# Optimization experiments

Measured on AMD Instinct MI355X. Metric: run time of the kernel, lower is better.

## Reference

```python
import jax, jax.numpy as jnp
import numpy as np

INV_SQRT2 = 0.7071067811865476  # ResidualLayer scale in GemNet
SILU_SCALE = 1.0 / 0.6          # ScaledSiLU scale factor


def scaled_silu(x):
    return jax.nn.silu(x) * SILU_SCALE


def setup_inputs() -> dict:
    key = jax.random.key(0)
    ks = jax.random.split(key, 9)
    E, A, D, NB = 200000, 10000, 256, 5  # edges, atoms, emb_size_edge, int_blocks+1

    def w(k, shape):
        fan_in = shape[0]
        return jax.random.normal(k, shape, jnp.float32) * (2.0 / fan_in) ** 0.5

    return {
        "x_cat": jax.random.normal(ks[0], (E, D * NB), jnp.float32),
        "edge_vec": jax.random.normal(ks[1], (E, 3), jnp.float32),
        "edge_idx": jax.random.randint(ks[2], (E,), 0, A),
        "W_in": w(ks[3], (D * NB, D)),
        "W_r1a": w(ks[4], (D, D)),
        "W_r1b": w(ks[5], (D, D)),
        "W_r2a": w(ks[6], (D, D)),
        "W_r2b": w(ks[7], (D, D)),
        "W_out": w(ks[8], (D, 1)),
        "n_atoms": A,
    }


def reference(x_cat, edge_vec, edge_idx, W_in, W_r1a, W_r1b, W_r2a, W_r2b, W_out, n_atoms):
    # out_mlp_F: Dense(in->emb) + 2 residual layers (all Dense are bias-free + ScaledSiLU)
    x = scaled_silu(x_cat @ W_in)                                   # [E, D]
    x = (x + scaled_silu(scaled_silu(x @ W_r1a) @ W_r1b)) * INV_SQRT2
    x = (x + scaled_silu(scaled_silu(x @ W_r2a) @ W_r2b)) * INV_SQRT2
    # out_forces: Dense(D -> 1, bias=False, no activation)
    F_st = x @ W_out                                                # [E, 1]
    # F_st_vec = F_st[:, :, None] * edge_vec[:, None, :] -> squeeze the size-1 dim
    F_vec = F_st * edge_vec                                         # [E, 3]
    # scatter_add over target atom index
    forces = jax.ops.segment_sum(F_vec, edge_idx, num_segments=n_atoms)  # [A, 3]
    return forces
```

## Files before the change

### kernel.cpp

```cpp
#include <hip/hip_runtime.h>

typedef __attribute__((ext_vector_type(4))) float f32x4;
typedef __attribute__((ext_vector_type(8))) __bf16 bf16x8;
typedef __attribute__((ext_vector_type(8))) unsigned short us8;
typedef unsigned short u16;

#define SSILU_SCALE (1.0f / 0.6f)
#define INV_SQRT2 0.70710678118654752f

__device__ __forceinline__ u16 f2bf(float f) {
    __bf16 h = (__bf16)f;
    return __builtin_bit_cast(u16, h);
}
__device__ __forceinline__ float bf2f(u16 h) {
    union { unsigned int u; float f; } v; v.u = ((unsigned int)h) << 16;
    return v.f;
}
__device__ __forceinline__ float ssilu(float x) {
    float e = __expf(-x);
    float s = __builtin_amdgcn_rcpf(1.0f + e);
    return x * s * SSILU_SCALE;
}

__global__ __launch_bounds__(256) void prep_kernel(
    const float* __restrict__ Win, const float* __restrict__ W1a,
    const float* __restrict__ W1b, const float* __restrict__ W2a,
    const float* __restrict__ W2b, u16* __restrict__ WinF,
    u16* __restrict__ Wfrag, float* __restrict__ out, int outN) {
    int i = blockIdx.x * 256 + threadIdx.x;
    if (i < 327680) {
        int e = i & 7, lane = (i >> 3) & 63, n = (i >> 9) & 3;
        int kk = (i >> 11) & 1, w = (i >> 12) & 3, kt = i >> 14;
        int lo = lane & 15, hi = lane >> 4;
        int k = kt * 64 + kk * 32 + hi * 8 + e;
        int col = w * 64 + n * 16 + lo;
        WinF[i] = f2bf(Win[k * 256 + col]);
        return;
    }
    int j = i - 327680;
    if (j < 262144) {
        int g = j >> 16, r = j & 65535;
        int chunk = r >> 9, within = r & 511;
        int lane = within >> 3, e = within & 7;
        int w = chunk >> 5, kk = (chunk >> 2) & 7, n = chunk & 3;
        int lo = lane & 15, hi = lane >> 4;
        int col = w * 64 + n * 16 + lo;
        int k = kk * 32 + hi * 8 + e;
        const float* W = (g == 0) ? W1a : (g == 1) ? W1b : (g == 2) ? W2a : W2b;
        Wfrag[j] = f2bf(W[k * 256 + col]);
        return;
    }
    int z = j - 262144;
    if (z < outN) out[z] = 0.0f;
}

__device__ __forceinline__ void gemm_lds(const char* AB, const u16* __restrict__ Wfw,
                                         int l, int lo, int hi, f32x4 acc[4][4]) {
#pragma unroll
    for (int m = 0; m < 4; m++)
#pragma unroll
        for (int n = 0; n < 4; n++) acc[m][n] = (f32x4){0.f, 0.f, 0.f, 0.f};
    bf16x8 bv[4];
#pragma unroll
    for (int n = 0; n < 4; n++)
        bv[n] = __builtin_bit_cast(bf16x8,
            *(const us8*)(Wfw + (size_t)n * 512 + l * 8));
#pragma unroll
    for (int kk = 0; kk < 8; ++kk) {
        int kbyte = kk * 64 + hi * 16;
        bf16x8 af[4], bvn[4];
#pragma unroll
        for (int m = 0; m < 4; m++) {
            int r = m * 16 + lo;
            af[m] = __builtin_bit_cast(bf16x8,
                *(const us8*)(AB + r * 512 + (kbyte ^ ((r & 7) << 4))));
        }
        if (kk < 7) {
#pragma unroll
            for (int n = 0; n < 4; n++)
                bvn[n] = __builtin_bit_cast(bf16x8,
                    *(const us8*)(Wfw + (size_t)((kk + 1) * 4 + n) * 512 + l * 8));
        }
#pragma unroll
        for (int m = 0; m < 4; m++)
#pragma unroll
            for (int n = 0; n < 4; n++)
                acc[m][n] = __builtin_amdgcn_mfma_f32_16x16x32_bf16(
                    af[m], bv[n], acc[m][n], 0, 0, 0);
        if (kk < 7) {
#pragma unroll
            for (int n = 0; n < 4; n++) bv[n] = bvn[n];
        }
    }
}

__global__ __launch_bounds__(256, 2) void fused_kernel(
    const float* __restrict__ A, const u16* __restrict__ WinF,
    const u16* __restrict__ Wfrag, const float* __restrict__ Wout,
    const float* __restrict__ evec, const int* __restrict__ eidx,
    float* __restrict__ out) {
    __shared__ u16 xb[64 * 256];
    __shared__ u16 tb[64 * 256];
    __shared__ float fpart[4][64];
    const int t = threadIdx.x, w = t >> 6, l = t & 63;
    const int lo = l & 15, hi = l >> 4;
    const long rowbase = (long)blockIdx.x * 64;
    char* xbB = (char*)xb;
    char* tbB = (char*)tb;
    char* As0 = (char*)tb;
    char* As1 = (char*)tb + 8192;

    f32x4 acc[4][4];
#pragma unroll
    for (int m = 0; m < 4; m++)
#pragma unroll
        for (int n = 0; n < 4; n++) acc[m][n] = (f32x4){0.f, 0.f, 0.f, 0.f};

    float4 va[2][2];
    auto LOADA = [&](int kb) {
#pragma unroll
        for (int c = 0; c < 2; ++c) {
            int idx = t + c * 256;
            int r = idx >> 3, k8 = (idx & 7) * 8;
            const float* s = A + (rowbase + r) * 1280 + kb + k8;
            va[c][0] = *(const float4*)s;
            va[c][1] = *(const float4*)(s + 4);
        }
    };
    auto WRITEA = [&](char* dst) {
#pragma unroll
        for (int c = 0; c < 2; ++c) {
            int idx = t + c * 256;
            int r = idx >> 3, k8 = (idx & 7) * 8;
            us8 p;
            p[0] = f2bf(va[c][0].x); p[1] = f2bf(va[c][0].y);
            p[2] = f2bf(va[c][0].z); p[3] = f2bf(va[c][0].w);
            p[4] = f2bf(va[c][1].x); p[5] = f2bf(va[c][1].y);
            p[6] = f2bf(va[c][1].z); p[7] = f2bf(va[c][1].w);
            *(us8*)(dst + r * 128 + ((k8 * 2) ^ ((r & 7) << 4))) = p;
        }
    };
    auto LOADB = [&](int kt, bf16x8 (&b)[8]) {
        const u16* base = WinF + kt * 16384 + w * 4096 + l * 8;
#pragma unroll
        for (int kk = 0; kk < 2; ++kk)
#pragma unroll
            for (int n = 0; n < 4; ++n)
                b[kk * 4 + n] = __builtin_bit_cast(bf16x8,
                    *(const us8*)(base + kk * 2048 + n * 512));
    };

    bf16x8 b0[8], b1[8];

    auto STEP = [&](int kt, const char* ABcur, char* ABnxt,
                    bf16x8 (&bc)[8], bf16x8 (&bn)[8]) {
        const bool more = (kt + 1 < 20);
        if (more) {
            LOADA((kt + 1) * 64);
            LOADB(kt + 1, bn);
        }
#pragma unroll
        for (int kk = 0; kk < 2; ++kk) {
            int kbyte = kk * 64 + hi * 16;
            bf16x8 af[4];
#pragma unroll
            for (int m = 0; m < 4; m++) {
                int r = m * 16 + lo;
                af[m] = __builtin_bit_cast(bf16x8,
                    *(const us8*)(ABcur + r * 128 + (kbyte ^ ((r & 7) << 4))));
            }
#pragma unroll
            for (int m = 0; m < 4; m++)
#pragma unroll
                for (int n = 0; n < 4; n++)
                    acc[m][n] = __builtin_amdgcn_mfma_f32_16x16x32_bf16(
                        af[m], bc[kk * 4 + n], acc[m][n], 0, 0, 0);
        }
        if (more) WRITEA(ABnxt);
        asm volatile("s_waitcnt lgkmcnt(0)" ::: "memory");
        __builtin_amdgcn_sched_barrier(0);
        __builtin_amdgcn_s_barrier();
    };

    LOADA(0);
    LOADB(0, b0);
    WRITEA(As0);
    asm volatile("s_waitcnt lgkmcnt(0)" ::: "memory");
    __builtin_amdgcn_s_barrier();

    for (int i = 0; i < 10; ++i) {
        STEP(2 * i,     As0, As1, b0, b1);
        STEP(2 * i + 1, As1, As0, b1, b0);
    }

#pragma unroll
    for (int m = 0; m < 4; m++)
#pragma unroll
        for (int n = 0; n < 4; n++)
#pragma unroll
            for (int j = 0; j < 4; j++) {
                int r = m * 16 + hi * 4 + j;
                int cc = w * 64 + n * 16 + lo;
                *(u16*)(xbB + r * 512 + ((cc * 2) ^ ((r & 7) << 4))) =
                    f2bf(ssilu(acc[m][n][j]));
            }
    __syncthreads();

    const u16* Wfw = Wfrag + w * 16384;

    gemm_lds(xbB, Wfw + 0 * 65536, l, lo, hi, acc);
#pragma unroll
    for (int m = 0; m < 4; m++)
#pragma unroll
        for (int n = 0; n < 4; n++)
#pragma unroll
            for (int j = 0; j < 4; j++) {
                int r = m * 16 + hi * 4 + j;
                int cc = w * 64 + n * 16 + lo;
                *(u16*)(tbB + r * 512 + ((cc * 2) ^ ((r & 7) << 4))) =
                    f2bf(ssilu(acc[m][n][j]));
            }
    __syncthreads();

    gemm_lds(tbB, Wfw + 1 * 65536, l, lo, hi, acc);
#pragma unroll
    for (int m = 0; m < 4; m++)
#pragma unroll
        for (int n = 0; n < 4; n++)
#pragma unroll
            for (int j = 0; j < 4; j++) {
                int r = m * 16 + hi * 4 + j;
                int cc = w * 64 + n * 16 + lo;
                char* p = xbB + r * 512 + ((cc * 2) ^ ((r & 7) << 4));
                float xn = (bf2f(*(u16*)p) + ssilu(acc[m][n][j])) * INV_SQRT2;
                *(u16*)p = f2bf(xn);
            }
    __syncthreads();

    gemm_lds(xbB, Wfw + 2 * 65536, l, lo, hi, acc);
#pragma unroll
    for (int m = 0; m < 4; m++)
#pragma unroll
        for (int n = 0; n < 4; n++)
#pragma unroll
            for (int j = 0; j < 4; j++) {
                int r = m * 16 + hi * 4 + j;
                int cc = w * 64 + n * 16 + lo;
                *(u16*)(tbB + r * 512 + ((cc * 2) ^ ((r & 7) << 4))) =
                    f2bf(ssilu(acc[m][n][j]));
            }
    __syncthreads();

    gemm_lds(tbB, Wfw + 3 * 65536, l, lo, hi, acc);
    float wo[4];
#pragma unroll
    for (int n = 0; n < 4; n++) wo[n] = Wout[w * 64 + n * 16 + lo];

    float part[4][4];
#pragma unroll
    for (int m = 0; m < 4; m++)
#pragma unroll
        for (int j = 0; j < 4; j++) part[m][j] = 0.f;
#pragma unroll
    for (int m = 0; m < 4; m++)
#pragma unroll
        for (int n = 0; n < 4; n++)
#pragma unroll
            for (int j = 0; j < 4; j++) {
                int r = m * 16 + hi * 4 + j;
                int cc = w * 64 + n * 16 + lo;
                const char* p = xbB + r * 512 + ((cc * 2) ^ ((r & 7) << 4));
                float xf = (bf2f(*(const u16*)p) + ssilu(acc[m][n][j])) * INV_SQRT2;
                part[m][j] += xf * wo[n];
            }
#pragma unroll
    for (int m = 0; m < 4; m++)
#pragma unroll
        for (int j = 0; j < 4; j++) {
            float v = part[m][j];
            v += __shfl_xor(v, 1);
            v += __shfl_xor(v, 2);
            v += __shfl_xor(v, 4);
            v += __shfl_xor(v, 8);
            if (lo == 0) fpart[w][m * 16 + hi * 4 + j] = v;
        }
    __syncthreads();

    if (t < 64) {
        int r = t;
        float F = fpart[0][r] + fpart[1][r] + fpart[2][r] + fpart[3][r];
        long e = rowbase + r;
        float vx = evec[e * 3 + 0], vy = evec[e * 3 + 1], vz = evec[e * 3 + 2];
        int a = eidx[e];
        atomicAdd(&out[a * 3 + 0], F * vx);
        atomicAdd(&out[a * 3 + 1], F * vy);
        atomicAdd(&out[a * 3 + 2], F * vz);
    }
}

extern "C" void kernel_launch(void* const* d_in, const int* in_sizes, int n_in,
                              void* d_out, int out_size, void* d_ws, size_t ws_size,
                              hipStream_t stream) {
    const float* x_cat = (const float*)d_in[0];
    const float* evec  = (const float*)d_in[1];
    const int*   eidx  = (const int*)d_in[2];
    const float* Win   = (const float*)d_in[3];
    const float* W1a   = (const float*)d_in[4];
    const float* W1b   = (const float*)d_in[5];
    const float* W2a   = (const float*)d_in[6];
    const float* W2b   = (const float*)d_in[7];
    const float* Wout  = (const float*)d_in[8];
    float* out = (float*)d_out;
    const int E = in_sizes[1] / 3;

    u16* WinF  = (u16*)d_ws;
    u16* Wfrag = WinF + 327680;

    int prepN = 327680 + 262144 + out_size;
    prep_kernel<<<(prepN + 255) / 256, 256, 0, stream>>>(
        Win, W1a, W1b, W2a, W2b, WinF, Wfrag, out, out_size);
    fused_kernel<<<E / 64, 256, 0, stream>>>(
        x_cat, WinF, Wfrag, Wout, evec, eidx, out);
}
```

Baseline: 406.2 us.

## Split fused MLP across 8 waves and deepen A-tile global prefetch

The fused kernel now uses 512 threads (8 waves) per 64-row tile, with each wave owning 32 output columns instead of 64. This halves accumulator and B-fragment registers per wave and adds more waves per CU to hide latency. The first GEMM's K loop is restructured into a software pipeline that keeps two A tiles in flight in registers ahead of the LDS write, hiding more of the global load latency. The trade-off is more waves contending for the same LDS tiles and barriers, and duplicated A-fragment LDS reads across the wave pairs.

```diff
diff --git a/kernel.cpp b/kernel.cpp
--- a/kernel.cpp
+++ b/kernel.cpp
@@ -54,111 +54,95 @@
     if (z < outN) out[z] = 0.0f;
 }
 
-__device__ __forceinline__ void gemm_lds(const char* AB, const u16* __restrict__ Wfw,
-                                         int l, int lo, int hi, f32x4 acc[4][4]) {
-#pragma unroll
-    for (int m = 0; m < 4; m++)
-#pragma unroll
-        for (int n = 0; n < 4; n++) acc[m][n] = (f32x4){0.f, 0.f, 0.f, 0.f};
-    bf16x8 bv[4];
-#pragma unroll
-    for (int n = 0; n < 4; n++)
-        bv[n] = __builtin_bit_cast(bf16x8,
-            *(const us8*)(Wfw + (size_t)n * 512 + l * 8));
+__device__ __forceinline__ void gemm_lds8(const char* AB, const u16* __restrict__ Wfw,
+                                          int swz, int hi, int lo, f32x4 acc[4][2]) {
+#pragma unroll
+    for (int m = 0; m < 4; m++)
+#pragma unroll
+        for (int n = 0; n < 2; n++) acc[m][n] = (f32x4){0.f, 0.f, 0.f, 0.f};
+    bf16x8 bv[2], bvn[2];
+#pragma unroll
+    for (int n = 0; n < 2; n++)
+        bv[n] = __builtin_bit_cast(bf16x8, *(const us8*)(Wfw + n * 512));
 #pragma unroll
     for (int kk = 0; kk < 8; ++kk) {
         int kbyte = kk * 64 + hi * 16;
-        bf16x8 af[4], bvn[4];
+        bf16x8 af[4];
 #pragma unroll
         for (int m = 0; m < 4; m++) {
             int r = m * 16 + lo;
             af[m] = __builtin_bit_cast(bf16x8,
-                *(const us8*)(AB + r * 512 + (kbyte ^ ((r & 7) << 4))));
+                *(const us8*)(AB + r * 512 + (kbyte ^ swz)));
         }
         if (kk < 7) {
 #pragma unroll
-            for (int n = 0; n < 4; n++)
+            for (int n = 0; n < 2; n++)
                 bvn[n] = __builtin_bit_cast(bf16x8,
-                    *(const us8*)(Wfw + (size_t)((kk + 1) * 4 + n) * 512 + l * 8));
+                    *(const us8*)(Wfw + (kk + 1) * 2048 + n * 512));
         }
 #pragma unroll
         for (int m = 0; m < 4; m++)
 #pragma unroll
-            for (int n = 0; n < 4; n++)
+            for (int n = 0; n < 2; n++)
                 acc[m][n] = __builtin_amdgcn_mfma_f32_16x16x32_bf16(
                     af[m], bv[n], acc[m][n], 0, 0, 0);
         if (kk < 7) {
 #pragma unroll
-            for (int n = 0; n < 4; n++) bv[n] = bvn[n];
-        }
-    }
-}
-
-__global__ __launch_bounds__(256, 2) void fused_kernel(
+            for (int n = 0; n < 2; n++) bv[n] = bvn[n];
+        }
+    }
+}
+
+__global__ __launch_bounds__(512, 4) void fused_kernel(
     const float* __restrict__ A, const u16* __restrict__ WinF,
     const u16* __restrict__ Wfrag, const float* __restrict__ Wout,
     const float* __restrict__ evec, const int* __restrict__ eidx,
     float* __restrict__ out) {
     __shared__ u16 xb[64 * 256];
     __shared__ u16 tb[64 * 256];
-    __shared__ float fpart[4][64];
+    __shared__ float fpart[8][64];
     const int t = threadIdx.x, w = t >> 6, l = t & 63;
     const int lo = l & 15, hi = l >> 4;
+    const int swz = (lo & 7) << 4;
     const long rowbase = (long)blockIdx.x * 64;
     char* xbB = (char*)xb;
     char* tbB = (char*)tb;
-    char* As0 = (char*)tb;
-    char* As1 = (char*)tb + 8192;
-
-    f32x4 acc[4][4];
-#pragma unroll
-    for (int m = 0; m < 4; m++)
-#pragma unroll
-        for (int n = 0; n < 4; n++) acc[m][n] = (f32x4){0.f, 0.f, 0.f, 0.f};
-
-    float4 va[2][2];
-    auto LOADA = [&](int kb) {
-#pragma unroll
-        for (int c = 0; c < 2; ++c) {
-            int idx = t + c * 256;
-            int r = idx >> 3, k8 = (idx & 7) * 8;
-            const float* s = A + (rowbase + r) * 1280 + kb + k8;
-            va[c][0] = *(const float4*)s;
-            va[c][1] = *(const float4*)(s + 4);
-        }
-    };
-    auto WRITEA = [&](char* dst) {
-#pragma unroll
-        for (int c = 0; c < 2; ++c) {
-            int idx = t + c * 256;
-            int r = idx >> 3, k8 = (idx & 7) * 8;
-            us8 p;
-            p[0] = f2bf(va[c][0].x); p[1] = f2bf(va[c][0].y);
-            p[2] = f2bf(va[c][0].z); p[3] = f2bf(va[c][0].w);
-            p[4] = f2bf(va[c][1].x); p[5] = f2bf(va[c][1].y);
-            p[6] = f2bf(va[c][1].z); p[7] = f2bf(va[c][1].w);
-            *(us8*)(dst + r * 128 + ((k8 * 2) ^ ((r & 7) << 4))) = p;
-        }
-    };
-    auto LOADB = [&](int kt, bf16x8 (&b)[8]) {
-        const u16* base = WinF + kt * 16384 + w * 4096 + l * 8;
+    char* As0 = tbB;
+    char* As1 = tbB + 8192;
+
+    f32x4 acc[4][2];
+#pragma unroll
+    for (int m = 0; m < 4; m++)
+#pragma unroll
+        for (int n = 0; n < 2; n++) acc[m][n] = (f32x4){0.f, 0.f, 0.f, 0.f};
+
+    const int ar = t >> 3, ak8 = (t & 7) * 8;
+    const int awz = ((ak8 * 2) ^ ((ar & 7) << 4));
+    float4 va0[2], va1[2];
+    auto LOADA = [&](int kb, float4* va) {
+        const float* s = A + (rowbase + ar) * 1280 + kb + ak8;
+        va[0] = *(const float4*)s;
+        va[1] = *(const float4*)(s + 4);
+    };
+    auto WRITEA = [&](char* dst, const float4* va) {
+        us8 p;
+        p[0] = f2bf(va[0].x); p[1] = f2bf(va[0].y);
+        p[2] = f2bf(va[0].z); p[3] = f2bf(va[0].w);
+        p[4] = f2bf(va[1].x); p[5] = f2bf(va[1].y);
+        p[6] = f2bf(va[1].z); p[7] = f2bf(va[1].w);
+        *(us8*)(dst + ar * 128 + awz) = p;
+    };
+    const u16* WinFw = WinF + (w >> 1) * 4096 + (w & 1) * 1024 + l * 8;
+    auto LOADB = [&](int kt, bf16x8 (&b)[4]) {
+        const u16* base = WinFw + kt * 16384;
 #pragma unroll
         for (int kk = 0; kk < 2; ++kk)
 #pragma unroll
-            for (int n = 0; n < 4; ++n)
-                b[kk * 4 + n] = __builtin_bit_cast(bf16x8,
+            for (int n = 0; n < 2; ++n)
+                b[kk * 2 + n] = __builtin_bit_cast(bf16x8,
                     *(const us8*)(base + kk * 2048 + n * 512));
     };
-
-    bf16x8 b0[8], b1[8];
-
-    auto STEP = [&](int kt, const char* ABcur, char* ABnxt,
-                    bf16x8 (&bc)[8], bf16x8 (&bn)[8]) {
-        const bool more = (kt + 1 < 20);
-        if (more) {
-            LOADA((kt + 1) * 64);
-            LOADB(kt + 1, bn);
-        }
+    auto MFMASTEP = [&](const char* AB, const bf16x8 (&bc)[4]) {
 #pragma unroll
         for (int kk = 0; kk < 2; ++kk) {
             int kbyte = kk * 64 + hi * 16;
@@ -167,94 +151,129 @@
             for (int m = 0; m < 4; m++) {
                 int r = m * 16 + lo;
                 af[m] = __builtin_bit_cast(bf16x8,
-                    *(const us8*)(ABcur + r * 128 + (kbyte ^ ((r & 7) << 4))));
+                    *(const us8*)(AB + r * 128 + (kbyte ^ swz)));
             }
 #pragma unroll
             for (int m = 0; m < 4; m++)
 #pragma unroll
-                for (int n = 0; n < 4; n++)
+                for (int n = 0; n < 2; n++)
                     acc[m][n] = __builtin_amdgcn_mfma_f32_16x16x32_bf16(
-                        af[m], bc[kk * 4 + n], acc[m][n], 0, 0, 0);
-        }
-        if (more) WRITEA(ABnxt);
+                        af[m], bc[kk * 2 + n], acc[m][n], 0, 0, 0);
+        }
+    };
+    auto FENCE = [&]() {
         asm volatile("s_waitcnt lgkmcnt(0)" ::: "memory");
         __builtin_amdgcn_sched_barrier(0);
         __builtin_amdgcn_s_barrier();
     };
 
-    LOADA(0);
+    bf16x8 b0[4], b1[4];
+
+    LOADA(0, va1);
+    WRITEA(As0, va1);
     LOADB(0, b0);
-    WRITEA(As0);
-    asm volatile("s_waitcnt lgkmcnt(0)" ::: "memory");
-    __builtin_amdgcn_s_barrier();
-
-    for (int i = 0; i < 10; ++i) {
-        STEP(2 * i,     As0, As1, b0, b1);
-        STEP(2 * i + 1, As1, As0, b1, b0);
-    }
-
-#pragma unroll
-    for (int m = 0; m < 4; m++)
-#pragma unroll
-        for (int n = 0; n < 4; n++)
-#pragma unroll
-            for (int j = 0; j < 4; j++) {
-                int r = m * 16 + hi * 4 + j;
-                int cc = w * 64 + n * 16 + lo;
+    LOADA(64, va0);
+    LOADA(128, va1);
+    FENCE();
+
+    for (int i = 0; i < 8; ++i) {
+        const int kt = 2 * i;
+        LOADB(kt + 1, b1);
+        __builtin_amdgcn_sched_barrier(0);
+        MFMASTEP(As0, b0);
+        WRITEA(As1, va0);
+        LOADA((kt + 3) * 64, va0);
+        FENCE();
+        LOADB(kt + 2, b0);
+        __builtin_amdgcn_sched_barrier(0);
+        MFMASTEP(As1, b1);
+        WRITEA(As0, va1);
+        LOADA((kt + 4) * 64, va1);
+        FENCE();
+    }
+    LOADB(17, b1);
+    __builtin_amdgcn_sched_barrier(0);
+    MFMASTEP(As0, b0);
+    WRITEA(As1, va0);
+    LOADA(19 * 64, va0);
+    FENCE();
+
+    LOADB(18, b0);
+    __builtin_amdgcn_sched_barrier(0);
+    MFMASTEP(As1, b1);
+    WRITEA(As0, va1);
+    FENCE();
+
+    LOADB(19, b1);
+    __builtin_amdgcn_sched_barrier(0);
+    MFMASTEP(As0, b0);
+    WRITEA(As1, va0);
+    FENCE();
+
+    MFMASTEP(As1, b1);
+
+#pragma unroll
+    for (int m = 0; m < 4; m++)
+#pragma unroll
+        for (int n = 0; n < 2; n++)
+#pragma unroll
+            for (int j = 0; j < 4; j++) {
+                int r = m * 16 + hi * 4 + j;
+                int cc = w * 32 + n * 16 + lo;
                 *(u16*)(xbB + r * 512 + ((cc * 2) ^ ((r & 7) << 4))) =
                     f2bf(ssilu(acc[m][n][j]));
             }
     __syncthreads();
 
-    const u16* Wfw = Wfrag + w * 16384;
-
-    gemm_lds(xbB, Wfw + 0 * 65536, l, lo, hi, acc);
-#pragma unroll
-    for (int m = 0; m < 4; m++)
-#pragma unroll
-        for (int n = 0; n < 4; n++)
-#pragma unroll
-            for (int j = 0; j < 4; j++) {
-                int r = m * 16 + hi * 4 + j;
-                int cc = w * 64 + n * 16 + lo;
+    const u16* Wfw = Wfrag + (w >> 1) * 16384 + (w & 1) * 1024 + l * 8;
+
+    gemm_lds8(xbB, Wfw + 0 * 65536, swz, hi, lo, acc);
+#pragma unroll
+    for (int m = 0; m < 4; m++)
+#pragma unroll
+        for (int n = 0; n < 2; n++)
+#pragma unroll
+            for (int j = 0; j < 4; j++) {
+                int r = m * 16 + hi * 4 + j;
+                int cc = w * 32 + n * 16 + lo;
                 *(u16*)(tbB + r * 512 + ((cc * 2) ^ ((r & 7) << 4))) =
                     f2bf(ssilu(acc[m][n][j]));
             }
     __syncthreads();
 
-    gemm_lds(tbB, Wfw + 1 * 65536, l, lo, hi, acc);
-#pragma unroll
-    for (int m = 0; m < 4; m++)
-#pragma unroll
-        for (int n = 0; n < 4; n++)
-#pragma unroll
-            for (int j = 0; j < 4; j++) {
-                int r = m * 16 + hi * 4 + j;
-                int cc = w * 64 + n * 16 + lo;
+    gemm_lds8(tbB, Wfw + 1 * 65536, swz, hi, lo, acc);
+#pragma unroll
+    for (int m = 0; m < 4; m++)
+#pragma unroll
+        for (int n = 0; n < 2; n++)
+#pragma unroll
+            for (int j = 0; j < 4; j++) {
+                int r = m * 16 + hi * 4 + j;
+                int cc = w * 32 + n * 16 + lo;
                 char* p = xbB + r * 512 + ((cc * 2) ^ ((r & 7) << 4));
                 float xn = (bf2f(*(u16*)p) + ssilu(acc[m][n][j])) * INV_SQRT2;
                 *(u16*)p = f2bf(xn);
             }
     __syncthreads();
 
-    gemm_lds(xbB, Wfw + 2 * 65536, l, lo, hi, acc);
-#pragma unroll
-    for (int m = 0; m < 4; m++)
-#pragma unroll
-        for (int n = 0; n < 4; n++)
-#pragma unroll
-            for (int j = 0; j < 4; j++) {
-                int r = m * 16 + hi * 4 + j;
-                int cc = w * 64 + n * 16 + lo;
+    gemm_lds8(xbB, Wfw + 2 * 65536, swz, hi, lo, acc);
+#pragma unroll
+    for (int m = 0; m < 4; m++)
+#pragma unroll
+        for (int n = 0; n < 2; n++)
+#pragma unroll
+            for (int j = 0; j < 4; j++) {
+                int r = m * 16 + hi * 4 + j;
+                int cc = w * 32 + n * 16 + lo;
                 *(u16*)(tbB + r * 512 + ((cc * 2) ^ ((r & 7) << 4))) =
                     f2bf(ssilu(acc[m][n][j]));
             }
     __syncthreads();
 
-    gemm_lds(tbB, Wfw + 3 * 65536, l, lo, hi, acc);
-    float wo[4];
-#pragma unroll
-    for (int n = 0; n < 4; n++) wo[n] = Wout[w * 64 + n * 16 + lo];
+    gemm_lds8(tbB, Wfw + 3 * 65536, swz, hi, lo, acc);
+    float wo[2];
+#pragma unroll
+    for (int n = 0; n < 2; n++) wo[n] = Wout[w * 32 + n * 16 + lo];
 
     float part[4][4];
 #pragma unroll
@@ -264,11 +283,11 @@
 #pragma unroll
     for (int m = 0; m < 4; m++)
 #pragma unroll
-        for (int n = 0; n < 4; n++)
-#pragma unroll
-            for (int j = 0; j < 4; j++) {
-                int r = m * 16 + hi * 4 + j;
-                int cc = w * 64 + n * 16 + lo;
+        for (int n = 0; n < 2; n++)
+#pragma unroll
+            for (int j = 0; j < 4; j++) {
+                int r = m * 16 + hi * 4 + j;
+                int cc = w * 32 + n * 16 + lo;
                 const char* p = xbB + r * 512 + ((cc * 2) ^ ((r & 7) << 4));
                 float xf = (bf2f(*(const u16*)p) + ssilu(acc[m][n][j])) * INV_SQRT2;
                 part[m][j] += xf * wo[n];
@@ -288,7 +307,8 @@
 
     if (t < 64) {
         int r = t;
-        float F = fpart[0][r] + fpart[1][r] + fpart[2][r] + fpart[3][r];
+        float F = fpart[0][r] + fpart[1][r] + fpart[2][r] + fpart[3][r] +
+                  fpart[4][r] + fpart[5][r] + fpart[6][r] + fpart[7][r];
         long e = rowbase + r;
         float vx = evec[e * 3 + 0], vy = evec[e * 3 + 1], vz = evec[e * 3 + 2];
         int a = eidx[e];
@@ -319,6 +339,6 @@
     int prepN = 327680 + 262144 + out_size;
     prep_kernel<<<(prepN + 255) / 256, 256, 0, stream>>>(
         Win, W1a, W1b, W2a, W2b, WinF, Wfrag, out, out_size);
-    fused_kernel<<<E / 64, 256, 0, stream>>>(
+    fused_kernel<<<E / 64, 512, 0, stream>>>(
         x_cat, WinF, Wfrag, Wout, evec, eidx, out);
 }
```

After: 423.3 us. +4.2%, slower.

## Halve rows per block to 32 and raise occupancy with finer-grained B prefetch

Applied to the files above, without the earlier changes.

Cuts the per-block edge tile from 64 to 32 rows, which halves the accumulators and LDS buffers. That lets launch bounds request 4 blocks per CU instead of 2. The first GEMM's pipeline now prefetches weight fragments per k-substep and loads A two tiles ahead. The aim is more latency hiding through higher occupancy. The cost is that each block reuses the weights over half as many rows, so per-block weight traffic from L2 roughly doubles relative to compute.

```diff
diff --git a/kernel.cpp b/kernel.cpp
--- a/kernel.cpp
+++ b/kernel.cpp
@@ -55,12 +55,12 @@
 }
 
 __device__ __forceinline__ void gemm_lds(const char* AB, const u16* __restrict__ Wfw,
-                                         int l, int lo, int hi, f32x4 acc[4][4]) {
-#pragma unroll
-    for (int m = 0; m < 4; m++)
+                                         int l, int lo, int hi, f32x4 acc[2][4]) {
+#pragma unroll
+    for (int m = 0; m < 2; m++)
 #pragma unroll
         for (int n = 0; n < 4; n++) acc[m][n] = (f32x4){0.f, 0.f, 0.f, 0.f};
-    bf16x8 bv[4];
+    bf16x8 bv[4], bvn[4];
 #pragma unroll
     for (int n = 0; n < 4; n++)
         bv[n] = __builtin_bit_cast(bf16x8,
@@ -68,9 +68,9 @@
 #pragma unroll
     for (int kk = 0; kk < 8; ++kk) {
         int kbyte = kk * 64 + hi * 16;
-        bf16x8 af[4], bvn[4];
-#pragma unroll
-        for (int m = 0; m < 4; m++) {
+        bf16x8 af[2];
+#pragma unroll
+        for (int m = 0; m < 2; m++) {
             int r = m * 16 + lo;
             af[m] = __builtin_bit_cast(bf16x8,
                 *(const us8*)(AB + r * 512 + (kbyte ^ ((r & 7) << 4))));
@@ -82,7 +82,7 @@
                     *(const us8*)(Wfw + (size_t)((kk + 1) * 4 + n) * 512 + l * 8));
         }
 #pragma unroll
-        for (int m = 0; m < 4; m++)
+        for (int m = 0; m < 2; m++)
 #pragma unroll
             for (int n = 0; n < 4; n++)
                 acc[m][n] = __builtin_amdgcn_mfma_f32_16x16x32_bf16(
@@ -94,107 +94,100 @@
     }
 }
 
-__global__ __launch_bounds__(256, 2) void fused_kernel(
+__global__ __launch_bounds__(256, 4) void fused_kernel(
     const float* __restrict__ A, const u16* __restrict__ WinF,
     const u16* __restrict__ Wfrag, const float* __restrict__ Wout,
     const float* __restrict__ evec, const int* __restrict__ eidx,
     float* __restrict__ out) {
-    __shared__ u16 xb[64 * 256];
-    __shared__ u16 tb[64 * 256];
-    __shared__ float fpart[4][64];
+    __shared__ u16 xb[32 * 256];
+    __shared__ u16 tb[32 * 256];
+    __shared__ float fpart[4][32];
     const int t = threadIdx.x, w = t >> 6, l = t & 63;
     const int lo = l & 15, hi = l >> 4;
-    const long rowbase = (long)blockIdx.x * 64;
+    const int swz = (lo & 7) << 4;
+    const long rowbase = (long)blockIdx.x * 32;
     char* xbB = (char*)xb;
     char* tbB = (char*)tb;
-    char* As0 = (char*)tb;
-    char* As1 = (char*)tb + 8192;
-
-    f32x4 acc[4][4];
-#pragma unroll
-    for (int m = 0; m < 4; m++)
+    char* As0 = tbB;
+    char* As1 = tbB + 4096;
+
+    f32x4 acc[2][4];
+#pragma unroll
+    for (int m = 0; m < 2; m++)
 #pragma unroll
         for (int n = 0; n < 4; n++) acc[m][n] = (f32x4){0.f, 0.f, 0.f, 0.f};
 
-    float4 va[2][2];
+    const int ar = t >> 3, ak8 = (t & 7) * 8;
+    const int awz = ((ak8 * 2) ^ ((ar & 7) << 4));
+    float4 va[2];
     auto LOADA = [&](int kb) {
-#pragma unroll
-        for (int c = 0; c < 2; ++c) {
-            int idx = t + c * 256;
-            int r = idx >> 3, k8 = (idx & 7) * 8;
-            const float* s = A + (rowbase + r) * 1280 + kb + k8;
-            va[c][0] = *(const float4*)s;
-            va[c][1] = *(const float4*)(s + 4);
-        }
+        const float* s = A + (rowbase + ar) * 1280 + kb + ak8;
+        va[0] = *(const float4*)s;
+        va[1] = *(const float4*)(s + 4);
     };
     auto WRITEA = [&](char* dst) {
-#pragma unroll
-        for (int c = 0; c < 2; ++c) {
-            int idx = t + c * 256;
-            int r = idx >> 3, k8 = (idx & 7) * 8;
-            us8 p;
-            p[0] = f2bf(va[c][0].x); p[1] = f2bf(va[c][0].y);
-            p[2] = f2bf(va[c][0].z); p[3] = f2bf(va[c][0].w);
-            p[4] = f2bf(va[c][1].x); p[5] = f2bf(va[c][1].y);
-            p[6] = f2bf(va[c][1].z); p[7] = f2bf(va[c][1].w);
-            *(us8*)(dst + r * 128 + ((k8 * 2) ^ ((r & 7) << 4))) = p;
-        }
-    };
-    auto LOADB = [&](int kt, bf16x8 (&b)[8]) {
-        const u16* base = WinF + kt * 16384 + w * 4096 + l * 8;
-#pragma unroll
-        for (int kk = 0; kk < 2; ++kk)
-#pragma unroll
-            for (int n = 0; n < 4; ++n)
-                b[kk * 4 + n] = __builtin_bit_cast(bf16x8,
-                    *(const us8*)(base + kk * 2048 + n * 512));
-    };
-
-    bf16x8 b0[8], b1[8];
-
-    auto STEP = [&](int kt, const char* ABcur, char* ABnxt,
-                    bf16x8 (&bc)[8], bf16x8 (&bn)[8]) {
-        const bool more = (kt + 1 < 20);
-        if (more) {
-            LOADA((kt + 1) * 64);
-            LOADB(kt + 1, bn);
-        }
-#pragma unroll
-        for (int kk = 0; kk < 2; ++kk) {
-            int kbyte = kk * 64 + hi * 16;
-            bf16x8 af[4];
-#pragma unroll
-            for (int m = 0; m < 4; m++) {
-                int r = m * 16 + lo;
-                af[m] = __builtin_bit_cast(bf16x8,
-                    *(const us8*)(ABcur + r * 128 + (kbyte ^ ((r & 7) << 4))));
-            }
-#pragma unroll
-            for (int m = 0; m < 4; m++)
-#pragma unroll
-                for (int n = 0; n < 4; n++)
-                    acc[m][n] = __builtin_amdgcn_mfma_f32_16x16x32_bf16(
-                        af[m], bc[kk * 4 + n], acc[m][n], 0, 0, 0);
-        }
-        if (more) WRITEA(ABnxt);
+        us8 p;
+        p[0] = f2bf(va[0].x); p[1] = f2bf(va[0].y);
+        p[2] = f2bf(va[0].z); p[3] = f2bf(va[0].w);
+        p[4] = f2bf(va[1].x); p[5] = f2bf(va[1].y);
+        p[6] = f2bf(va[1].z); p[7] = f2bf(va[1].w);
+        *(us8*)(dst + ar * 128 + awz) = p;
+    };
+    const u16* WinFw = WinF + w * 4096 + l * 8;
+    auto LOADB = [&](int kt, int kk, bf16x8 (&b)[4]) {
+        const u16* base = WinFw + kt * 16384 + kk * 2048;
+#pragma unroll
+        for (int n = 0; n < 4; ++n)
+            b[n] = __builtin_bit_cast(bf16x8, *(const us8*)(base + n * 512));
+    };
+    auto MFMA_KK = [&](const char* AB, int kk, const bf16x8 (&bc)[4]) {
+        int kbyte = kk * 64 + hi * 16;
+        bf16x8 af[2];
+#pragma unroll
+        for (int m = 0; m < 2; m++) {
+            int r = m * 16 + lo;
+            af[m] = __builtin_bit_cast(bf16x8,
+                *(const us8*)(AB + r * 128 + (kbyte ^ swz)));
+        }
+#pragma unroll
+        for (int m = 0; m < 2; m++)
+#pragma unroll
+            for (int n = 0; n < 4; n++)
+                acc[m][n] = __builtin_amdgcn_mfma_f32_16x16x32_bf16(
+                    af[m], bc[n], acc[m][n], 0, 0, 0);
+    };
+    auto FENCE = [&]() {
         asm volatile("s_waitcnt lgkmcnt(0)" ::: "memory");
         __builtin_amdgcn_sched_barrier(0);
         __builtin_amdgcn_s_barrier();
     };
 
+    bf16x8 bc[4], bn[4];
+
     LOADA(0);
-    LOADB(0, b0);
     WRITEA(As0);
-    asm volatile("s_waitcnt lgkmcnt(0)" ::: "memory");
-    __builtin_amdgcn_s_barrier();
+    LOADB(0, 0, bc);
+    LOADA(64);
+    FENCE();
+
+    auto STEP = [&](int kt, const char* AScur, char* ASnxt) {
+        const bool more = (kt < 19);
+        LOADB(kt, 1, bn);
+        MFMA_KK(AScur, 0, bc);
+        if (more) LOADB(kt + 1, 0, bc);
+        MFMA_KK(AScur, 1, bn);
+        if (more) WRITEA(ASnxt);
+        if (kt <= 17) LOADA((kt + 2) * 64);
+        FENCE();
+    };
 
     for (int i = 0; i < 10; ++i) {
-        STEP(2 * i,     As0, As1, b0, b1);
-        STEP(2 * i + 1, As1, As0, b1, b0);
-    }
-
-#pragma unroll
-    for (int m = 0; m < 4; m++)
+        STEP(2 * i,     As0, As1);
+        STEP(2 * i + 1, As1, As0);
+    }
+
+#pragma unroll
+    for (int m = 0; m < 2; m++)
 #pragma unroll
         for (int n = 0; n < 4; n++)
 #pragma unroll
@@ -210,7 +203,7 @@
 
     gemm_lds(xbB, Wfw + 0 * 65536, l, lo, hi, acc);
 #pragma unroll
-    for (int m = 0; m < 4; m++)
+    for (int m = 0; m < 2; m++)
 #pragma unroll
         for (int n = 0; n < 4; n++)
 #pragma unroll
@@ -224,7 +217,7 @@
 
     gemm_lds(tbB, Wfw + 1 * 65536, l, lo, hi, acc);
 #pragma unroll
-    for (int m = 0; m < 4; m++)
+    for (int m = 0; m < 2; m++)
 #pragma unroll
         for (int n = 0; n < 4; n++)
 #pragma unroll
@@ -239,7 +232,7 @@
 
     gemm_lds(xbB, Wfw + 2 * 65536, l, lo, hi, acc);
 #pragma unroll
-    for (int m = 0; m < 4; m++)
+    for (int m = 0; m < 2; m++)
 #pragma unroll
         for (int n = 0; n < 4; n++)
 #pragma unroll
@@ -256,13 +249,13 @@
 #pragma unroll
     for (int n = 0; n < 4; n++) wo[n] = Wout[w * 64 + n * 16 + lo];
 
-    float part[4][4];
-#pragma unroll
-    for (int m = 0; m < 4; m++)
+    float part[2][4];
+#pragma unroll
+    for (int m = 0; m < 2; m++)
 #pragma unroll
         for (int j = 0; j < 4; j++) part[m][j] = 0.f;
 #pragma unroll
-    for (int m = 0; m < 4; m++)
+    for (int m = 0; m < 2; m++)
 #pragma unroll
         for (int n = 0; n < 4; n++)
 #pragma unroll
@@ -274,7 +267,7 @@
                 part[m][j] += xf * wo[n];
             }
 #pragma unroll
-    for (int m = 0; m < 4; m++)
+    for (int m = 0; m < 2; m++)
 #pragma unroll
         for (int j = 0; j < 4; j++) {
             float v = part[m][j];
@@ -286,7 +279,7 @@
         }
     __syncthreads();
 
-    if (t < 64) {
+    if (t < 32) {
         int r = t;
         float F = fpart[0][r] + fpart[1][r] + fpart[2][r] + fpart[3][r];
         long e = rowbase + r;
@@ -319,6 +312,6 @@
     int prepN = 327680 + 262144 + out_size;
     prep_kernel<<<(prepN + 255) / 256, 256, 0, stream>>>(
         Win, W1a, W1b, W2a, W2b, WinF, Wfrag, out, out_size);
-    fused_kernel<<<E / 64, 256, 0, stream>>>(
+    fused_kernel<<<E / 32, 256, 0, stream>>>(
         x_cat, WinF, Wfrag, Wout, evec, eidx, out);
 }
```

Measured after the change: 520.6 us. 28.1% more time.

## Double K-tile to 128 and prefetch A two steps ahead in input GEMM

Applied to the files above, without the earlier changes.

The first GEMM (1280->256) now stages 128-wide K tiles of the fp32 input into LDS instead of 64-wide ones. This halves the number of barriers, from 20 to 10. Global loads of A are issued two stages ahead, and the weight fragments are split into half-tile loads that interleave with the MFMA halves. The goal is better hiding of HBM latency for the dominant input stream, at the cost of more registers (va[4][2]) and more LDS per buffer, which may pressure occupancy at 2 blocks/CU.

```diff
diff --git a/kernel.cpp b/kernel.cpp
--- a/kernel.cpp
+++ b/kernel.cpp
@@ -60,7 +60,7 @@
     for (int m = 0; m < 4; m++)
 #pragma unroll
         for (int n = 0; n < 4; n++) acc[m][n] = (f32x4){0.f, 0.f, 0.f, 0.f};
-    bf16x8 bv[4];
+    bf16x8 bv[4], bvn[4];
 #pragma unroll
     for (int n = 0; n < 4; n++)
         bv[n] = __builtin_bit_cast(bf16x8,
@@ -68,7 +68,7 @@
 #pragma unroll
     for (int kk = 0; kk < 8; ++kk) {
         int kbyte = kk * 64 + hi * 16;
-        bf16x8 af[4], bvn[4];
+        bf16x8 af[4];
 #pragma unroll
         for (int m = 0; m < 4; m++) {
             int r = m * 16 + lo;
@@ -104,11 +104,12 @@
     __shared__ float fpart[4][64];
     const int t = threadIdx.x, w = t >> 6, l = t & 63;
     const int lo = l & 15, hi = l >> 4;
+    const int swz = (lo & 7) << 4;
     const long rowbase = (long)blockIdx.x * 64;
     char* xbB = (char*)xb;
     char* tbB = (char*)tb;
-    char* As0 = (char*)tb;
-    char* As1 = (char*)tb + 8192;
+    char* As0 = tbB;
+    char* As1 = tbB + 16384;
 
     f32x4 acc[4][4];
 #pragma unroll
@@ -116,12 +117,12 @@
 #pragma unroll
         for (int n = 0; n < 4; n++) acc[m][n] = (f32x4){0.f, 0.f, 0.f, 0.f};
 
-    float4 va[2][2];
+    float4 va[4][2];
     auto LOADA = [&](int kb) {
 #pragma unroll
-        for (int c = 0; c < 2; ++c) {
+        for (int c = 0; c < 4; ++c) {
             int idx = t + c * 256;
-            int r = idx >> 3, k8 = (idx & 7) * 8;
+            int r = idx >> 4, k8 = (idx & 15) * 8;
             const float* s = A + (rowbase + r) * 1280 + kb + k8;
             va[c][0] = *(const float4*)s;
             va[c][1] = *(const float4*)(s + 4);
@@ -129,68 +130,75 @@
     };
     auto WRITEA = [&](char* dst) {
 #pragma unroll
-        for (int c = 0; c < 2; ++c) {
+        for (int c = 0; c < 4; ++c) {
             int idx = t + c * 256;
-            int r = idx >> 3, k8 = (idx & 7) * 8;
+            int r = idx >> 4, k8 = (idx & 15) * 8;
             us8 p;
             p[0] = f2bf(va[c][0].x); p[1] = f2bf(va[c][0].y);
             p[2] = f2bf(va[c][0].z); p[3] = f2bf(va[c][0].w);
             p[4] = f2bf(va[c][1].x); p[5] = f2bf(va[c][1].y);
             p[6] = f2bf(va[c][1].z); p[7] = f2bf(va[c][1].w);
-            *(us8*)(dst + r * 128 + ((k8 * 2) ^ ((r & 7) << 4))) = p;
-        }
-    };
+            *(us8*)(dst + r * 256 + ((k8 * 2) ^ ((r & 7) << 4))) = p;
+        }
+    };
+    const u16* WinFw = WinF + w * 4096 + l * 8;
     auto LOADB = [&](int kt, bf16x8 (&b)[8]) {
-        const u16* base = WinF + kt * 16384 + w * 4096 + l * 8;
-#pragma unroll
-        for (int kk = 0; kk < 2; ++kk)
+        const u16* base = WinFw + kt * 16384;
+#pragma unroll
+        for (int kkL = 0; kkL < 2; ++kkL)
 #pragma unroll
             for (int n = 0; n < 4; ++n)
-                b[kk * 4 + n] = __builtin_bit_cast(bf16x8,
-                    *(const us8*)(base + kk * 2048 + n * 512));
-    };
-
-    bf16x8 b0[8], b1[8];
-
-    auto STEP = [&](int kt, const char* ABcur, char* ABnxt,
-                    bf16x8 (&bc)[8], bf16x8 (&bn)[8]) {
-        const bool more = (kt + 1 < 20);
-        if (more) {
-            LOADA((kt + 1) * 64);
-            LOADB(kt + 1, bn);
-        }
-#pragma unroll
-        for (int kk = 0; kk < 2; ++kk) {
-            int kbyte = kk * 64 + hi * 16;
+                b[kkL * 4 + n] = __builtin_bit_cast(bf16x8,
+                    *(const us8*)(base + kkL * 2048 + n * 512));
+    };
+    auto MFMA_HALF = [&](const char* AB, int half, const bf16x8 (&b)[8]) {
+#pragma unroll
+        for (int kkL = 0; kkL < 2; ++kkL) {
+            int kbyte = (half * 2 + kkL) * 64 + hi * 16;
             bf16x8 af[4];
 #pragma unroll
             for (int m = 0; m < 4; m++) {
                 int r = m * 16 + lo;
                 af[m] = __builtin_bit_cast(bf16x8,
-                    *(const us8*)(ABcur + r * 128 + (kbyte ^ ((r & 7) << 4))));
+                    *(const us8*)(AB + r * 256 + (kbyte ^ swz)));
             }
 #pragma unroll
             for (int m = 0; m < 4; m++)
 #pragma unroll
                 for (int n = 0; n < 4; n++)
                     acc[m][n] = __builtin_amdgcn_mfma_f32_16x16x32_bf16(
-                        af[m], bc[kk * 4 + n], acc[m][n], 0, 0, 0);
-        }
-        if (more) WRITEA(ABnxt);
+                        af[m], b[kkL * 4 + n], acc[m][n], 0, 0, 0);
+        }
+    };
+    auto FENCE = [&]() {
         asm volatile("s_waitcnt lgkmcnt(0)" ::: "memory");
         __builtin_amdgcn_sched_barrier(0);
         __builtin_amdgcn_s_barrier();
     };
 
+    bf16x8 bc[8], bn[8];
+
     LOADA(0);
-    LOADB(0, b0);
     WRITEA(As0);
-    asm volatile("s_waitcnt lgkmcnt(0)" ::: "memory");
-    __builtin_amdgcn_s_barrier();
-
-    for (int i = 0; i < 10; ++i) {
-        STEP(2 * i,     As0, As1, b0, b1);
-        STEP(2 * i + 1, As1, As0, b1, b0);
+    LOADB(0, bc);
+    LOADA(128);
+    FENCE();
+
+    auto STEP = [&](int s, const char* AScur, char* ASnxt) {
+        const bool more = (s < 9);
+        LOADB(2 * s + 1, bn);
+        __builtin_amdgcn_sched_barrier(0);
+        MFMA_HALF(AScur, 0, bc);
+        if (more) LOADB(2 * s + 2, bc);
+        MFMA_HALF(AScur, 1, bn);
+        if (more) WRITEA(ASnxt);
+        if (s <= 7) LOADA((s + 2) * 128);
+        FENCE();
+    };
+
+    for (int i = 0; i < 5; ++i) {
+        STEP(2 * i,     As0, As1);
+        STEP(2 * i + 1, As1, As0);
     }
 
 #pragma unroll
```

Result: faster. 390.4 us (-3.9%).
